# Kernel optimization log

Measured on AMD Instinct MI355X. Metric: run time of the kernel, lower is better.

Reference implementation:

```python
import jax, jax.numpy as jnp
import numpy as np

BN_EPS = 1e-3  # O-CNN default bn_eps


def setup_inputs() -> dict:
    key = jax.random.key(0)
    k1, k2, k3 = jax.random.split(key, 3)
    N, Cin, Cout, K = 100000, 32, 32, 27  # nodes, channels, 3x3x3 taps
    data_in = jax.random.normal(k1, (1, Cin, N, 1), dtype=jnp.float32)
    neigh = jax.random.randint(k2, (N, K), 0, N, dtype=jnp.int32)
    weight = jax.random.normal(k3, (K, Cin, Cout), dtype=jnp.float32) * 0.05
    gamma = jnp.ones((Cout,), dtype=jnp.float32)
    beta = jnp.zeros((Cout,), dtype=jnp.float32)
    return {"data_in": data_in, "neigh": neigh, "weight": weight,
            "gamma": gamma, "beta": beta}


def reference(data_in, neigh, weight, gamma, beta):
    # data_in: [1, Cin, N, 1] -> x: [N, Cin]
    x = data_in[0, :, :, 0].T
    # Octree conv: gather 27 neighbor features per node, then small matmul.
    col = x[neigh]                                   # [N, 27, Cin] (irregular gather)
    y = jnp.einsum('nkc,kcd->nd', col, weight)       # [N, Cout]
    # BatchNorm2d in training mode: stats over the N (spatial) axis.
    mean = jnp.mean(y, axis=0)
    var = jnp.mean(jnp.square(y - mean), axis=0)     # biased variance, as BN uses
    yn = (y - mean) * jax.lax.rsqrt(var + BN_EPS) * gamma + beta
    # back to O-CNN layout [1, Cout, N, 1]
    return yn.T[None, :, :, None]
```

## Files before the change

kernel.cpp:

```cpp
#include <hip/hip_runtime.h>


#define KK 27
#define PT 14

typedef short bf16x8 __attribute__((ext_vector_type(8)));
typedef float f32x4  __attribute__((ext_vector_type(4)));

__device__ inline unsigned short f2bf(float f) {
    unsigned u = __float_as_uint(f);
    unsigned r = u + 0x7fffu + ((u >> 16) & 1u);
    return (unsigned short)(r >> 16);
}

__global__ __launch_bounds__(256) void prep_k(const float* __restrict__ in,
                                              const float* __restrict__ w,
                                              unsigned short* __restrict__ xLo,
                                              unsigned short* __restrict__ xHi,
                                              unsigned short* __restrict__ wP0,
                                              unsigned short* __restrict__ wP1,
                                              float* __restrict__ tot,
                                              int N, int nxblk) {
    __shared__ float tile[32][33];
    const int b = blockIdx.x;
    if (b < nxblk) {
        int n0 = b * 32;
        int tx = threadIdx.x & 31;
        int ty = threadIdx.x >> 5;
#pragma unroll
        for (int c = ty; c < 32; c += 8) {
            int n = n0 + tx;
            tile[c][tx] = (n < N) ? in[(long)c * N + n] : 0.f;
        }
        __syncthreads();
#pragma unroll
        for (int nn = ty; nn < 32; nn += 8) {
            int n = n0 + nn;
            if (n < N) {
                unsigned short v = f2bf(tile[tx][nn]);
                if (tx < 16) xLo[(long)n * 16 + tx]        = v;
                else         xHi[(long)n * 16 + (tx - 16)] = v;
            }
        }
        if (b == 0 && threadIdx.x < 32) {
            int t = threadIdx.x;
            if (t < 16) xLo[(long)N * 16 + t]        = 0;
            else        xHi[(long)N * 16 + (t - 16)] = 0;
        }
    } else {
        int t = b - nxblk;
        for (int i = threadIdx.x; i < 1024; i += 256) {
            int cout = i >> 5, k32 = i & 31;
            int tap = 2 * t + (k32 >> 4);
            int c   = k32 & 15;
            unsigned short lo = 0, hi = 0;
            if (tap < KK) {
                lo = f2bf(w[tap * 1024 + c * 32 + cout]);
                hi = f2bf(w[tap * 1024 + (c + 16) * 32 + cout]);
            }
            wP0[t * 1024 + cout * 32 + k32] = lo;
            wP1[t * 1024 + cout * 32 + k32] = hi;
        }
        if (t == 0) {
            for (int i = threadIdx.x; i < 32 * 64; i += 256) tot[i] = 0.f;
        }
    }
}

__global__ __launch_bounds__(64, 4) void conv_k(const unsigned short* __restrict__ xLo,
                                                const unsigned short* __restrict__ xHi,
                                                const int* __restrict__ neigh,
                                                const unsigned short* __restrict__ wP0,
                                                const unsigned short* __restrict__ wP1,
                                                float* __restrict__ y,
                                                float* __restrict__ tot,
                                                int N) {
    __shared__ float ct[32][33];

    const int L    = threadIdx.x;
    const int r16  = L & 15;
    const int quad = L >> 4;
    const int tapsel = quad >> 1;
    const int off8   = (quad & 1) * 8;
    const int base = blockIdx.x * 32;
    const int n0 = base + r16;
    const int n1 = base + 16 + r16;
    const bool v0 = (n0 < N), v1 = (n1 < N);
    const long nb0 = (long)(v0 ? n0 : 0) * KK;
    const long nb1 = (long)(v1 ? n1 : 0) * KK;

    f32x4 acc00 = {0.f, 0.f, 0.f, 0.f};
    f32x4 acc01 = acc00, acc10 = acc00, acc11 = acc00;

    auto ldidx = [&](long nb, bool v, int kq) -> int {
        int kc = (kq < KK) ? kq : (KK - 1);
        int j  = __builtin_nontemporal_load(neigh + nb + kc);
        return (v && kq < KK) ? j : N;
    };

#pragma unroll 1
    for (int ph = 0; ph < 2; ++ph) {
        const unsigned short* __restrict__ xp = ph ? xHi : xLo;
        const unsigned short* __restrict__ wp = ph ? wP1 : wP0;

        int ia = ldidx(nb0, v0, tapsel);
        int ib = ldidx(nb1, v1, tapsel);
        int ja = ldidx(nb0, v0, 2 + tapsel);
        int jb = ldidx(nb1, v1, 2 + tapsel);

        bf16x8 a0 = *(const bf16x8*)(xp + (long)ia * 16 + off8);
        bf16x8 a1 = *(const bf16x8*)(xp + (long)ib * 16 + off8);
        bf16x8 b0 = *(const bf16x8*)(wp + r16 * 32 + quad * 8);
        bf16x8 b1 = *(const bf16x8*)(wp + (16 + r16) * 32 + quad * 8);

#pragma unroll 1
        for (int t = 0; t < PT; ++t) {
            bf16x8 na0, na1, pb0, pb1;
            if (t < PT - 1) {
                na0 = *(const bf16x8*)(xp + (long)ja * 16 + off8);
                na1 = *(const bf16x8*)(xp + (long)jb * 16 + off8);
                const unsigned short* wn = wp + (t + 1) * 1024;
                pb0 = *(const bf16x8*)(wn + r16 * 32 + quad * 8);
                pb1 = *(const bf16x8*)(wn + (16 + r16) * 32 + quad * 8);
                ja = ldidx(nb0, v0, 2 * (t + 2) + tapsel);
                jb = ldidx(nb1, v1, 2 * (t + 2) + tapsel);
            }

            acc00 = __builtin_amdgcn_mfma_f32_16x16x32_bf16(a0, b0, acc00, 0, 0, 0);
            acc01 = __builtin_amdgcn_mfma_f32_16x16x32_bf16(a0, b1, acc01, 0, 0, 0);
            acc10 = __builtin_amdgcn_mfma_f32_16x16x32_bf16(a1, b0, acc10, 0, 0, 0);
            acc11 = __builtin_amdgcn_mfma_f32_16x16x32_bf16(a1, b1, acc11, 0, 0, 0);

            if (t < PT - 1) {
                a0 = na0;
                a1 = na1;
                b0 = pb0;
                b1 = pb1;
            }
        }
    }

    float s0 = 0.f, q0 = 0.f, s1 = 0.f, q1 = 0.f;
#pragma unroll
    for (int r = 0; r < 4; ++r) {
        s0 += acc00[r] + acc10[r];
        q0 += acc00[r] * acc00[r] + acc10[r] * acc10[r];
        s1 += acc01[r] + acc11[r];
        q1 += acc01[r] * acc01[r] + acc11[r] * acc11[r];
    }
#pragma unroll
    for (int off = 16; off < 64; off <<= 1) {
        s0 += __shfl_xor(s0, off, 64);
        q0 += __shfl_xor(q0, off, 64);
        s1 += __shfl_xor(s1, off, 64);
        q1 += __shfl_xor(q1, off, 64);
    }
    const int stripe = blockIdx.x & 31;
    if (L < 16) {
        float* tb = tot + stripe * 64;
        atomicAdd(&tb[L],      s0);
        atomicAdd(&tb[L + 16], s1);
        atomicAdd(&tb[L + 32], q0);
        atomicAdd(&tb[L + 48], q1);
    }

#pragma unroll
    for (int r = 0; r < 4; ++r) {
        ct[quad * 4 + r][r16]           = acc00[r];
        ct[quad * 4 + r][16 + r16]      = acc01[r];
        ct[16 + quad * 4 + r][r16]      = acc10[r];
        ct[16 + quad * 4 + r][16 + r16] = acc11[r];
    }
    __syncthreads();
    const int node = L & 31;
    const int half = L >> 5;
    const int gn = base + node;
    if (gn < N) {
#pragma unroll
        for (int i = 0; i < 16; ++i) {
            const int cout = i * 2 + half;
            __builtin_nontemporal_store(ct[node][cout], y + (long)cout * N + gn);
        }
    }
}

__global__ __launch_bounds__(256) void norm_k(float* __restrict__ y,
                                              const float* __restrict__ tot,
                                              const float* __restrict__ gamma,
                                              const float* __restrict__ beta, int N) {
    const int d = blockIdx.y;
    float sm = 0.f, sq = 0.f;
#pragma unroll
    for (int s = 0; s < 32; ++s) {
        sm += tot[s * 64 + d];
        sq += tot[s * 64 + 32 + d];
    }
    const float mean = sm / (float)N;
    const float var  = sq / (float)N - mean * mean;
    const float sc   = gamma[d] * rsqrtf(var + 1e-3f);
    const float sh   = beta[d] - mean * sc;

    int i = blockIdx.x * blockDim.x + threadIdx.x;
    int base = i * 4;
    if (base + 3 < N) {
        float4* p = (float4*)(y + (long)d * N + base);
        float4 v = *p;
        v.x = fmaf(v.x, sc, sh);
        v.y = fmaf(v.y, sc, sh);
        v.z = fmaf(v.z, sc, sh);
        v.w = fmaf(v.w, sc, sh);
        *p = v;
    } else if (base < N) {
        for (int t = base; t < N; ++t) y[(long)d * N + t] = fmaf(y[(long)d * N + t], sc, sh);
    }
}

extern "C" void kernel_launch(void* const* d_in, const int* in_sizes, int n_in,
                              void* d_out, int out_size, void* d_ws, size_t ws_size,
                              hipStream_t stream) {
    const float* data_in = (const float*)d_in[0];
    const int*   neigh   = (const int*)d_in[1];
    const float* weight  = (const float*)d_in[2];
    const float* gamma   = (const float*)d_in[3];
    const float* beta    = (const float*)d_in[4];
    float* out = (float*)d_out;

    const int N = in_sizes[1] / KK;
    const int nxblk = (N + 31) / 32;
    const int nblk  = (N + 31) / 32;

    char* ws = (char*)d_ws;
    size_t halfBytes = (size_t)(N + 1) * 32;
    unsigned short* xLo = (unsigned short*)ws;
    unsigned short* xHi = (unsigned short*)(ws + halfBytes);
    unsigned short* wP0 = (unsigned short*)(ws + 2 * halfBytes);
    unsigned short* wP1 = wP0 + PT * 1024;
    float* tot = (float*)((char*)(wP1 + PT * 1024));

    prep_k<<<nxblk + PT, 256, 0, stream>>>(data_in, weight, xLo, xHi, wP0, wP1, tot, N, nxblk);
    conv_k<<<nblk, 64, 0, stream>>>(xLo, xHi, neigh, wP0, wP1, out, tot, N);
    dim3 ngrid(((N + 3) / 4 + 255) / 256, 32);
    norm_k<<<ngrid, 256, 0, stream>>>(out, tot, gamma, beta, N);
}
```

Before: 153.1 us.

## Fuse conv and batchnorm into one persistent kernel with grid barriers

Replaces the separate conv and norm kernels with one persistent kernel using 256-thread blocks (four waves, one 32-node tile each), capped at 1024 blocks. A software grid barrier between the lo and hi channel phases keeps waves in lockstep so the gathered half-buffers stay cache-resident. A final barrier lets the same blocks read the global statistics and normalize their own tiles in place. This removes one kernel launch and the separate normalization pass, but adds spin-wait barriers that need every block resident at once and can deadlock if they are not.

```diff
diff --git a/kernel.cpp b/kernel.cpp
--- a/kernel.cpp
+++ b/kernel.cpp
@@ -1,8 +1,8 @@
 #include <hip/hip_runtime.h>
-
 
 #define KK 27
 #define PT 14
+#define SC_AGENT __HIP_MEMORY_SCOPE_AGENT
 
 typedef short bf16x8 __attribute__((ext_vector_type(8)));
 typedef float f32x4  __attribute__((ext_vector_type(4)));
@@ -20,6 +20,7 @@
                                               unsigned short* __restrict__ wP0,
                                               unsigned short* __restrict__ wP1,
                                               float* __restrict__ tot,
+                                              int* __restrict__ bar,
                                               int N, int nxblk) {
     __shared__ float tile[32][33];
     const int b = blockIdx.x;
@@ -63,155 +64,205 @@
         }
         if (t == 0) {
             for (int i = threadIdx.x; i < 32 * 64; i += 256) tot[i] = 0.f;
-        }
-    }
-}
-
-__global__ __launch_bounds__(64, 4) void conv_k(const unsigned short* __restrict__ xLo,
-                                                const unsigned short* __restrict__ xHi,
-                                                const int* __restrict__ neigh,
-                                                const unsigned short* __restrict__ wP0,
-                                                const unsigned short* __restrict__ wP1,
-                                                float* __restrict__ y,
-                                                float* __restrict__ tot,
-                                                int N) {
-    __shared__ float ct[32][33];
-
-    const int L    = threadIdx.x;
-    const int r16  = L & 15;
-    const int quad = L >> 4;
-    const int tapsel = quad >> 1;
-    const int off8   = (quad & 1) * 8;
-    const int base = blockIdx.x * 32;
-    const int n0 = base + r16;
-    const int n1 = base + 16 + r16;
-    const bool v0 = (n0 < N), v1 = (n1 < N);
-    const long nb0 = (long)(v0 ? n0 : 0) * KK;
-    const long nb1 = (long)(v1 ? n1 : 0) * KK;
-
-    f32x4 acc00 = {0.f, 0.f, 0.f, 0.f};
-    f32x4 acc01 = acc00, acc10 = acc00, acc11 = acc00;
-
+            for (int i = threadIdx.x; i < 16 * 1024; i += 256) bar[i] = 0;
+        }
+    }
+}
+
+__device__ __forceinline__ void rendezvous(int* slab, int nblk) {
+    __syncthreads();
+    if (threadIdx.x == 0) {
+        const int g = blockIdx.x & 15;
+        const int expect = ((nblk - 1 - g) >> 4) + 1;
+        int* flag = slab + 512 + g * 16;
+        bool release = false;
+        if (__hip_atomic_fetch_add(slab + g * 16, 1, __ATOMIC_RELAXED, SC_AGENT)
+            == expect - 1) {
+            if (__hip_atomic_fetch_add(slab + 256, 1, __ATOMIC_RELAXED, SC_AGENT)
+                == 15) release = true;
+        }
+        if (release) {
+#pragma unroll
+            for (int i = 0; i < 16; ++i)
+                __hip_atomic_store(slab + 512 + i * 16, 1, __ATOMIC_RELAXED, SC_AGENT);
+        } else {
+            while (__hip_atomic_load(flag, __ATOMIC_RELAXED, SC_AGENT) == 0)
+                __builtin_amdgcn_s_sleep(64);
+        }
+    }
+    __syncthreads();
+}
+
+__device__ __forceinline__ void conv_phase(const unsigned short* __restrict__ xp,
+                                           const unsigned short* __restrict__ wp,
+                                           const int* __restrict__ neigh,
+                                           long nb0, long nb1, bool v0, bool v1,
+                                           int r16, int quad, int tapsel, int off8,
+                                           int N, f32x4& acc00, f32x4& acc01,
+                                           f32x4& acc10, f32x4& acc11) {
     auto ldidx = [&](long nb, bool v, int kq) -> int {
         int kc = (kq < KK) ? kq : (KK - 1);
         int j  = __builtin_nontemporal_load(neigh + nb + kc);
         return (v && kq < KK) ? j : N;
     };
+    int ia = ldidx(nb0, v0, tapsel);
+    int ib = ldidx(nb1, v1, tapsel);
+    int ja = ldidx(nb0, v0, 2 + tapsel);
+    int jb = ldidx(nb1, v1, 2 + tapsel);
+
+    bf16x8 a0 = *(const bf16x8*)(xp + (long)ia * 16 + off8);
+    bf16x8 a1 = *(const bf16x8*)(xp + (long)ib * 16 + off8);
+    bf16x8 b0 = *(const bf16x8*)(wp + r16 * 32 + quad * 8);
+    bf16x8 b1 = *(const bf16x8*)(wp + (16 + r16) * 32 + quad * 8);
 
 #pragma unroll 1
-    for (int ph = 0; ph < 2; ++ph) {
-        const unsigned short* __restrict__ xp = ph ? xHi : xLo;
-        const unsigned short* __restrict__ wp = ph ? wP1 : wP0;
-
-        int ia = ldidx(nb0, v0, tapsel);
-        int ib = ldidx(nb1, v1, tapsel);
-        int ja = ldidx(nb0, v0, 2 + tapsel);
-        int jb = ldidx(nb1, v1, 2 + tapsel);
-
-        bf16x8 a0 = *(const bf16x8*)(xp + (long)ia * 16 + off8);
-        bf16x8 a1 = *(const bf16x8*)(xp + (long)ib * 16 + off8);
-        bf16x8 b0 = *(const bf16x8*)(wp + r16 * 32 + quad * 8);
-        bf16x8 b1 = *(const bf16x8*)(wp + (16 + r16) * 32 + quad * 8);
-
-#pragma unroll 1
-        for (int t = 0; t < PT; ++t) {
-            bf16x8 na0, na1, pb0, pb1;
-            if (t < PT - 1) {
-                na0 = *(const bf16x8*)(xp + (long)ja * 16 + off8);
-                na1 = *(const bf16x8*)(xp + (long)jb * 16 + off8);
-                const unsigned short* wn = wp + (t + 1) * 1024;
-                pb0 = *(const bf16x8*)(wn + r16 * 32 + quad * 8);
-                pb1 = *(const bf16x8*)(wn + (16 + r16) * 32 + quad * 8);
-                ja = ldidx(nb0, v0, 2 * (t + 2) + tapsel);
-                jb = ldidx(nb1, v1, 2 * (t + 2) + tapsel);
-            }
-
-            acc00 = __builtin_amdgcn_mfma_f32_16x16x32_bf16(a0, b0, acc00, 0, 0, 0);
-            acc01 = __builtin_amdgcn_mfma_f32_16x16x32_bf16(a0, b1, acc01, 0, 0, 0);
-            acc10 = __builtin_amdgcn_mfma_f32_16x16x32_bf16(a1, b0, acc10, 0, 0, 0);
-            acc11 = __builtin_amdgcn_mfma_f32_16x16x32_bf16(a1, b1, acc11, 0, 0, 0);
-
-            if (t < PT - 1) {
-                a0 = na0;
-                a1 = na1;
-                b0 = pb0;
-                b1 = pb1;
-            }
-        }
-    }
-
-    float s0 = 0.f, q0 = 0.f, s1 = 0.f, q1 = 0.f;
-#pragma unroll
-    for (int r = 0; r < 4; ++r) {
-        s0 += acc00[r] + acc10[r];
-        q0 += acc00[r] * acc00[r] + acc10[r] * acc10[r];
-        s1 += acc01[r] + acc11[r];
-        q1 += acc01[r] * acc01[r] + acc11[r] * acc11[r];
-    }
-#pragma unroll
-    for (int off = 16; off < 64; off <<= 1) {
-        s0 += __shfl_xor(s0, off, 64);
-        q0 += __shfl_xor(q0, off, 64);
-        s1 += __shfl_xor(s1, off, 64);
-        q1 += __shfl_xor(q1, off, 64);
-    }
-    const int stripe = blockIdx.x & 31;
-    if (L < 16) {
-        float* tb = tot + stripe * 64;
-        atomicAdd(&tb[L],      s0);
-        atomicAdd(&tb[L + 16], s1);
-        atomicAdd(&tb[L + 32], q0);
-        atomicAdd(&tb[L + 48], q1);
-    }
-
-#pragma unroll
-    for (int r = 0; r < 4; ++r) {
-        ct[quad * 4 + r][r16]           = acc00[r];
-        ct[quad * 4 + r][16 + r16]      = acc01[r];
-        ct[16 + quad * 4 + r][r16]      = acc10[r];
-        ct[16 + quad * 4 + r][16 + r16] = acc11[r];
+    for (int t = 0; t < PT; ++t) {
+        bf16x8 na0, na1, pb0, pb1;
+        if (t < PT - 1) {
+            na0 = *(const bf16x8*)(xp + (long)ja * 16 + off8);
+            na1 = *(const bf16x8*)(xp + (long)jb * 16 + off8);
+            const unsigned short* wn = wp + (t + 1) * 1024;
+            pb0 = *(const bf16x8*)(wn + r16 * 32 + quad * 8);
+            pb1 = *(const bf16x8*)(wn + (16 + r16) * 32 + quad * 8);
+            ja = ldidx(nb0, v0, 2 * (t + 2) + tapsel);
+            jb = ldidx(nb1, v1, 2 * (t + 2) + tapsel);
+        }
+        acc00 = __builtin_amdgcn_mfma_f32_16x16x32_bf16(a0, b0, acc00, 0, 0, 0);
+        acc01 = __builtin_amdgcn_mfma_f32_16x16x32_bf16(a0, b1, acc01, 0, 0, 0);
+        acc10 = __builtin_amdgcn_mfma_f32_16x16x32_bf16(a1, b0, acc10, 0, 0, 0);
+        acc11 = __builtin_amdgcn_mfma_f32_16x16x32_bf16(a1, b1, acc11, 0, 0, 0);
+        if (t < PT - 1) {
+            a0 = na0; a1 = na1; b0 = pb0; b1 = pb1;
+        }
+    }
+}
+
+__global__ __launch_bounds__(256, 4) void convnorm_k(const unsigned short* __restrict__ xLo,
+                                                     const unsigned short* __restrict__ xHi,
+                                                     const int* __restrict__ neigh,
+                                                     const unsigned short* __restrict__ wP0,
+                                                     const unsigned short* __restrict__ wP1,
+                                                     const float* __restrict__ gamma,
+                                                     const float* __restrict__ beta,
+                                                     float* __restrict__ y,
+                                                     float* __restrict__ tot,
+                                                     int* __restrict__ bar,
+                                                     int N) {
+    __shared__ float ct[4][32][33];
+
+    const int tid    = threadIdx.x;
+    const int L      = tid & 63;
+    const int wv     = tid >> 6;
+    const int r16    = L & 15;
+    const int quad   = L >> 4;
+    const int tapsel = quad >> 1;
+    const int off8   = (quad & 1) * 8;
+    const int ntiles = (N + 31) / 32;
+    const int step   = (int)gridDim.x * 4;
+    const int iters  = (ntiles + step - 1) / step;
+
+    for (int it = 0; it < iters; ++it) {
+        const int tile_id = blockIdx.x * 4 + wv + it * step;
+        const int base = tile_id * 32;
+        const int n0 = base + r16;
+        const int n1 = base + 16 + r16;
+        const bool v0 = (n0 < N), v1 = (n1 < N);
+        const long nb0 = (long)(v0 ? n0 : 0) * KK;
+        const long nb1 = (long)(v1 ? n1 : 0) * KK;
+
+        f32x4 acc00 = {0.f, 0.f, 0.f, 0.f};
+        f32x4 acc01 = acc00, acc10 = acc00, acc11 = acc00;
+
+        conv_phase(xLo, wP0, neigh, nb0, nb1, v0, v1, r16, quad, tapsel, off8, N,
+                   acc00, acc01, acc10, acc11);
+
+        rendezvous(bar + it * 1024, (int)gridDim.x);
+
+        conv_phase(xHi, wP1, neigh, nb0, nb1, v0, v1, r16, quad, tapsel, off8, N,
+                   acc00, acc01, acc10, acc11);
+
+        float s0 = 0.f, q0 = 0.f, s1 = 0.f, q1 = 0.f;
+#pragma unroll
+        for (int r = 0; r < 4; ++r) {
+            s0 += acc00[r] + acc10[r];
+            q0 += acc00[r] * acc00[r] + acc10[r] * acc10[r];
+            s1 += acc01[r] + acc11[r];
+            q1 += acc01[r] * acc01[r] + acc11[r] * acc11[r];
+        }
+#pragma unroll
+        for (int off = 16; off < 64; off <<= 1) {
+            s0 += __shfl_xor(s0, off, 64);
+            q0 += __shfl_xor(q0, off, 64);
+            s1 += __shfl_xor(s1, off, 64);
+            q1 += __shfl_xor(q1, off, 64);
+        }
+        const int stripe = tile_id & 31;
+        if (L < 16) {
+            float* tb = tot + stripe * 64;
+            atomicAdd(&tb[L],      s0);
+            atomicAdd(&tb[L + 16], s1);
+            atomicAdd(&tb[L + 32], q0);
+            atomicAdd(&tb[L + 48], q1);
+        }
+
+#pragma unroll
+        for (int r = 0; r < 4; ++r) {
+            ct[wv][quad * 4 + r][r16]           = acc00[r];
+            ct[wv][quad * 4 + r][16 + r16]      = acc01[r];
+            ct[wv][16 + quad * 4 + r][r16]      = acc10[r];
+            ct[wv][16 + quad * 4 + r][16 + r16] = acc11[r];
+        }
+        const int node = L & 31;
+        const int half = L >> 5;
+        const int gn = base + node;
+        if (gn < N) {
+#pragma unroll
+            for (int i = 0; i < 16; ++i) {
+                const int cout = i * 2 + half;
+                __builtin_nontemporal_store(ct[wv][node][cout], y + (long)cout * N + gn);
+            }
+        }
+    }
+
+    rendezvous(bar + 15 * 1024, (int)gridDim.x);
+
+    float* sums = (float*)ct;
+    if (tid < 64) {
+        float v = 0.f;
+#pragma unroll
+        for (int s = 0; s < 32; ++s)
+            v += __hip_atomic_load(&tot[s * 64 + tid], __ATOMIC_RELAXED, SC_AGENT);
+        sums[tid] = v;
     }
     __syncthreads();
-    const int node = L & 31;
-    const int half = L >> 5;
-    const int gn = base + node;
-    if (gn < N) {
-#pragma unroll
-        for (int i = 0; i < 16; ++i) {
-            const int cout = i * 2 + half;
-            __builtin_nontemporal_store(ct[node][cout], y + (long)cout * N + gn);
-        }
-    }
-}
-
-__global__ __launch_bounds__(256) void norm_k(float* __restrict__ y,
-                                              const float* __restrict__ tot,
-                                              const float* __restrict__ gamma,
-                                              const float* __restrict__ beta, int N) {
-    const int d = blockIdx.y;
-    float sm = 0.f, sq = 0.f;
-#pragma unroll
-    for (int s = 0; s < 32; ++s) {
-        sm += tot[s * 64 + d];
-        sq += tot[s * 64 + 32 + d];
-    }
-    const float mean = sm / (float)N;
-    const float var  = sq / (float)N - mean * mean;
-    const float sc   = gamma[d] * rsqrtf(var + 1e-3f);
-    const float sh   = beta[d] - mean * sc;
-
-    int i = blockIdx.x * blockDim.x + threadIdx.x;
-    int base = i * 4;
-    if (base + 3 < N) {
-        float4* p = (float4*)(y + (long)d * N + base);
-        float4 v = *p;
-        v.x = fmaf(v.x, sc, sh);
-        v.y = fmaf(v.y, sc, sh);
-        v.z = fmaf(v.z, sc, sh);
-        v.w = fmaf(v.w, sc, sh);
-        *p = v;
-    } else if (base < N) {
-        for (int t = base; t < N; ++t) y[(long)d * N + t] = fmaf(y[(long)d * N + t], sc, sh);
+
+    {
+        const float invN = 1.f / (float)N;
+        const int cout = tid >> 3;
+        const int l8   = tid & 7;
+        const float mean = sums[cout] * invN;
+        const float var  = sums[32 + cout] * invN - mean * mean;
+        const float sc   = gamma[cout] * rsqrtf(var + 1e-3f);
+        const float sh   = beta[cout] - mean * sc;
+        for (int it = 0; it < iters; ++it) {
+            const long rb = ((long)blockIdx.x * 4 + (long)it * step) * 32;
+#pragma unroll
+            for (int j = 0; j < 4; ++j) {
+                const long nb = rb + l8 * 16 + j * 4;
+                float* yp = y + (long)cout * N + nb;
+                if (nb + 3 < N) {
+                    float4 v = *(float4*)yp;
+                    v.x = fmaf(v.x, sc, sh);
+                    v.y = fmaf(v.y, sc, sh);
+                    v.z = fmaf(v.z, sc, sh);
+                    v.w = fmaf(v.w, sc, sh);
+                    *(float4*)yp = v;
+                } else if (nb < N) {
+                    for (long t = nb; t < N; ++t)
+                        y[(long)cout * N + t] = fmaf(y[(long)cout * N + t], sc, sh);
+                }
+            }
+        }
     }
 }
 
@@ -225,9 +276,12 @@
     const float* beta    = (const float*)d_in[4];
     float* out = (float*)d_out;
 
-    const int N = in_sizes[1] / KK;
-    const int nxblk = (N + 31) / 32;
-    const int nblk  = (N + 31) / 32;
+    int N = in_sizes[1] / KK;
+    const int nxblk  = (N + 31) / 32;
+    const int ntiles = (N + 31) / 32;
+    int nblk = (ntiles + 3) / 4;
+    if (nblk > 1024) nblk = 1024;
+    if (nblk < 1) nblk = 1;
 
     char* ws = (char*)d_ws;
     size_t halfBytes = (size_t)(N + 1) * 32;
@@ -235,10 +289,11 @@
     unsigned short* xHi = (unsigned short*)(ws + halfBytes);
     unsigned short* wP0 = (unsigned short*)(ws + 2 * halfBytes);
     unsigned short* wP1 = wP0 + PT * 1024;
-    float* tot = (float*)((char*)(wP1 + PT * 1024));
-
-    prep_k<<<nxblk + PT, 256, 0, stream>>>(data_in, weight, xLo, xHi, wP0, wP1, tot, N, nxblk);
-    conv_k<<<nblk, 64, 0, stream>>>(xLo, xHi, neigh, wP0, wP1, out, tot, N);
-    dim3 ngrid(((N + 3) / 4 + 255) / 256, 32);
-    norm_k<<<ngrid, 256, 0, stream>>>(out, tot, gamma, beta, N);
-}
+    float* tot = (float*)(wP1 + PT * 1024);
+    int*   bar = (int*)(tot + 2048);
+
+    prep_k<<<nxblk + PT, 256, 0, stream>>>(data_in, weight, xLo, xHi, wP0, wP1,
+                                           tot, bar, N, nxblk);
+    convnorm_k<<<dim3(nblk), dim3(256), 0, stream>>>(xLo, xHi, neigh, wP0, wP1,
+                                                     gamma, beta, out, tot, bar, N);
+}
```

New measurement: 167.3 us. 1.09x slower.
